# Optimization experiments

Hardware: AMD Instinct MI355X
Metric: run time of the kernel (lower is better)

The kernel has to match this reference:

```python
import jax, jax.numpy as jnp
import numpy as np
from jax import lax

NX, NY = 512, 512          # grid
NCHAN, NOPEN = 4, 16        # channels / MLP hidden
NT = 8                      # timesteps
CG_ITERS = 10               # fixed CG iterations (CG.pcg source unavailable)
H = 1.0 / 16.0
DT = 1.0 / 64.0
N = NX * NY


def apply_lap(u):
    """Weighted 5-point Laplacian (Sigma=1, Neumann BC) / h^2. u: (ny, nx)."""
    dx = u[:, 1:] - u[:, :-1]            # (ny, nx-1)
    dy = u[1:, :] - u[:-1, :]            # (ny-1, nx)
    out = jnp.zeros_like(u)
    out = out.at[:, :-1].add(-dx).at[:, 1:].add(dx)
    out = out.at[:-1, :].add(-dy).at[1:, :].add(dy)
    return out * (1.0 / (H * H))


def cg_solve(b, gamma):
    """Solve (L + gamma*I) x = b with x0=0, fixed CG iterations. b: (ny, nx)."""
    A = lambda v: apply_lap(v) + gamma * v
    x = jnp.zeros_like(b)
    r = b
    p = r
    rs = jnp.sum(r * r)

    def body(carry, _):
        x, r, p, rs = carry
        Ap = A(p)
        alpha = rs / jnp.sum(p * Ap)
        x = x + alpha * p
        r = r - alpha * Ap
        rs_new = jnp.sum(r * r)
        p = r + (rs_new / rs) * p
        return (x, r, p, rs_new), None

    (x, _, _, _), _ = lax.scan(body, (x, r, p, rs), None, length=CG_ITERS)
    return x


def setup_inputs() -> dict:
    key = jax.random.key(0)
    k0, k1, k2, k3 = jax.random.split(key, 4)
    U0 = jax.random.normal(k0, (N, NCHAN), dtype=jnp.float32)
    # xavier_normal_ init for the three MLP weights
    def xavier(k, shape):
        std = float(np.sqrt(2.0 / (shape[0] + shape[1])))
        return jax.random.normal(k, shape, dtype=jnp.float32) * std
    K1 = xavier(k1, (NCHAN, NOPEN))
    K2 = xavier(k2, (NOPEN, NOPEN))
    K3 = xavier(k3, (NOPEN, NCHAN))
    scale = jnp.array([0.001, 0.01, 0.1, 1.0], dtype=jnp.float32)
    return {"U0": U0, "scale": scale, "K1": K1, "K2": K2, "K3": K3}


def reference(U0, scale, K1, K2, K3):
    gamma = 1.0 / (scale * DT)  # (NCHAN,)

    def step(U, _):
        # implicit diffusion per channel: solve (L + g I) u_new = g * u
        grids = U.T.reshape(NCHAN, NY, NX)                       # (C, ny, nx)
        sol = jax.vmap(lambda g, gm: cg_solve(gm * g, gm))(grids, gamma)
        U = sol.reshape(NCHAN, N).T                              # (N, C)
        # reaction: 3-layer tanh MLP
        U = U + DT * jnp.tanh(jnp.tanh(jnp.tanh(U @ K1) @ K2) @ K3)
        return U, None

    U, _ = lax.scan(step, U0, None, length=NT)
    return U
```

## Files before the change

### kernel.cpp

```cpp
#include <hip/hip_runtime.h>

#define NXg 512
#define NYg 512
#define NNg (NXg*NYg)
#define TPB 512
#define NBT 256
#define NSTEPS 8
#define CGIT 10
#define DTf (1.0f/64.0f)
#define H2I 256.0f

#define RELGEN 4096
#define SCAL   4098
#define CTRL_FLOATS 8192
#define W_OFF(par,c) (CTRL_FLOATS + ((par)*4+(c))*NNg)
#define B_OFF(c)     (CTRL_FLOATS + (8+(c))*NNg)

__device__ __forceinline__ int ld_flag(int* p){
  return __hip_atomic_load(p, __ATOMIC_RELAXED, __HIP_MEMORY_SCOPE_AGENT);
}
__device__ __forceinline__ void st_flag(int* p, int v){
  __hip_atomic_store(p, v, __ATOMIC_RELAXED, __HIP_MEMORY_SCOPE_AGENT);
}
union F2U { unsigned long long u; float2 f; };
__device__ __forceinline__ float2 ldg2(float* p){
  F2U t; t.u = __hip_atomic_load((unsigned long long*)p, __ATOMIC_RELAXED, __HIP_MEMORY_SCOPE_AGENT);
  return t.f;
}
__device__ __forceinline__ void stg2(float* p, float2 v){
  F2U t; t.f = v;
  __hip_atomic_store((unsigned long long*)p, t.u, __ATOMIC_RELAXED, __HIP_MEMORY_SCOPE_AGENT);
}

__device__ __forceinline__ void mlp_all(const float* sW, const float* vv, float* o){
  float h1[16];
  #pragma unroll
  for (int h=0;h<16;++h)
    h1[h] = tanhf(vv[0]*sW[h]+vv[1]*sW[16+h]+vv[2]*sW[32+h]+vv[3]*sW[48+h]);
  o[0]=o[1]=o[2]=o[3]=0.f;
  #pragma unroll
  for (int j=0;j<16;++j){
    float s=0.f;
    #pragma unroll
    for (int h=0;h<16;++h) s += h1[h]*sW[64+16*h+j];
    const float t = tanhf(s);
    o[0]+=t*sW[320+4*j+0]; o[1]+=t*sW[320+4*j+1];
    o[2]+=t*sW[320+4*j+2]; o[3]+=t*sW[320+4*j+3];
  }
}

__global__ void __launch_bounds__(TPB)
drk(const float* __restrict__ U0, const float* __restrict__ scale,
    const float* __restrict__ K1, const float* __restrict__ K2,
    const float* __restrict__ K3, float* __restrict__ out,
    float* __restrict__ ws)
{
  __shared__ float sW[384];
  __shared__ float sP[2][4][NXg];
  __shared__ float wRed[8][12];
  __shared__ float sAB[8];

  const int tid=threadIdx.x, bid=blockIdx.x;
  const int r    = tid>>8;
  const int lane = tid&63;
  const int wv   = tid>>6;
  const int c2   = (tid&255)*2;
  const int grow = bid*2 + r;
  const int cell0= grow*NXg + c2;
  const bool hUp = (r==0) && (grow>0);
  const bool hDn = (r==1) && (grow<NYg-1);
  const bool hasHalo = hUp || hDn;
  const int hrow = (r==0) ? (grow-1) : (grow+1);

  if (tid < 384){
    float w;
    if (tid < 64)       w = K1[tid];
    else if (tid < 320) w = K2[tid-64];
    else                w = K3[tid-320];
    sW[tid]=w;
  }
  __syncthreads();

  int* wsi = (int*)ws;
  float gam[4];
  #pragma unroll
  for (int c=0;c<4;++c) gam[c] = 1.0f/(scale[c]*DTf);

  float xnew[2][4];
  {
    const float4 u0 = ((const float4*)U0)[cell0];
    const float4 u1 = ((const float4*)U0)[cell0+1];
    xnew[0][0]=u0.x; xnew[0][1]=u0.y; xnew[0][2]=u0.z; xnew[0][3]=u0.w;
    xnew[1][0]=u1.x; xnew[1][1]=u1.y; xnew[1][2]=u1.z; xnew[1][3]=u1.w;
  }

  float rs_prev[4]={0,0,0,0}, pAp_prev[4]={0,0,0,0};

  for (int step=0; step<NSTEPS; ++step){
    float rr[2][4], xx[2][4], pp[2][4], Ap[2][4];
    float rh[2][4], Aph[2][4];
    #pragma unroll
    for (int c=0;c<4;++c)
    #pragma unroll
    for (int k=0;k<2;++k){
      rr[k][c] = gam[c]*xnew[k][c];
      xx[k][c]=0.f; pp[k][c]=0.f; Ap[k][c]=0.f; Aph[k][c]=0.f; rh[k][c]=0.f;
    }
    if (hasHalo){
      if (step==0){
        const float4 h0 = ((const float4*)U0)[hrow*NXg + c2];
        const float4 h1 = ((const float4*)U0)[hrow*NXg + c2+1];
        rh[0][0]=gam[0]*h0.x; rh[0][1]=gam[1]*h0.y; rh[0][2]=gam[2]*h0.z; rh[0][3]=gam[3]*h0.w;
        rh[1][0]=gam[0]*h1.x; rh[1][1]=gam[1]*h1.y; rh[1][2]=gam[2]*h1.z; rh[1][3]=gam[3]*h1.w;
      } else {
        #pragma unroll
        for (int c=0;c<4;++c){
          const float2 h = ldg2(ws + B_OFF(c) + hrow*NXg + c2);
          rh[0][c]=h.x; rh[1][c]=h.y;
        }
      }
    }

    for (int it=0; it<CGIT; ++it){
      const int tgt = step*11 + it + 1;
      const int par = it&1;

      #pragma unroll
      for (int k=0;k<2;++k)
      #pragma unroll
      for (int c=0;c<4;++c) sP[r][c][c2+k] = rr[k][c];
      __syncthreads();

      float w[2][4];
      #pragma unroll
      for (int c=0;c<4;++c)
      #pragma unroll
      for (int k=0;k<2;++k){
        const int col = c2+k;
        const float u = rr[k][c];
        float s = 0.f;
        if (r==1) s += u - sP[0][c][col]; else if (grow>0)     s += u - rh[k][c];
        if (r==0) s += u - sP[1][c][col]; else if (grow<NYg-1) s += u - rh[k][c];
        if (col > 0)     s += u - ((k==1) ? rr[0][c] : sP[r][c][col-1]);
        if (col < NXg-1) s += u - ((k==0) ? rr[1][c] : sP[r][c][col+1]);
        w[k][c] = s*H2I + gam[c]*u;
      }
      if (hasHalo && it < CGIT-1){
        #pragma unroll
        for (int c=0;c<4;++c)
          stg2(ws + W_OFF(par,c) + grow*NXg + c2, make_float2(w[0][c],w[1][c]));
      }

      float m12[12];
      #pragma unroll
      for (int c=0;c<4;++c){
        float rs_l=0.f, rw_l=0.f, rA_l=0.f;
        #pragma unroll
        for (int k=0;k<2;++k){
          rs_l += rr[k][c]*rr[k][c];
          rw_l += rr[k][c]*w[k][c];
          rA_l += rr[k][c]*Ap[k][c];
        }
        m12[c]=rs_l; m12[4+c]=rw_l; m12[8+c]=rA_l;
      }
      #pragma unroll
      for (int m=0;m<12;++m){
        float v=m12[m];
        #pragma unroll
        for (int off=32; off; off>>=1) v += __shfl_xor(v, off);
        m12[m]=v;
      }
      if (lane==0){
        #pragma unroll
        for (int m=0;m<12;++m) wRed[wv][m]=m12[m];
      }
      asm volatile("s_waitcnt vmcnt(0)" ::: "memory");
      __syncthreads();

      if (wv==0){
        float s=0.f;
        if (lane<12){
          #pragma unroll
          for (int q=0;q<8;++q) s += wRed[q][lane];
        }
        const float s0 = __shfl(s, 2*lane);
        const float s1 = __shfl(s, 2*lane+1);
        if (lane<6) stg2(ws + bid*16 + 2*lane, make_float2(s0,s1));
        asm volatile("s_waitcnt vmcnt(0)" ::: "memory");
        if (lane==0) st_flag(&wsi[bid*16+12], tgt);
      }

      if (bid==0 && tid<64){
        const int b0 = tid*4;
        int ok=0;
        while(!ok){
          int m=1;
          #pragma unroll
          for (int j=0;j<4;++j) m &= (ld_flag(&wsi[(b0+j)*16+12]) >= tgt);
          ok=__all(m);
          if(!ok) __builtin_amdgcn_s_sleep(1);
        }
        float mm[12];
        #pragma unroll
        for (int m=0;m<12;++m) mm[m]=0.f;
        #pragma unroll
        for (int j=0;j<4;++j)
          #pragma unroll
          for (int t=0;t<6;++t){
            const float2 v = ldg2(ws + (b0+j)*16 + 2*t);
            mm[2*t] += v.x; mm[2*t+1] += v.y;
          }
        #pragma unroll
        for (int m=0;m<12;++m){
          float v=mm[m];
          #pragma unroll
          for (int off=32; off; off>>=1) v += __shfl_xor(v, off);
          mm[m]=v;
        }
        float aR[4], bR[4];
        #pragma unroll
        for (int c=0;c<4;++c){
          const float rsv=mm[c], rwv=mm[4+c], rAv=mm[8+c];
          const float bet = (it==0) ? 0.f
                          : ((rs_prev[c] > 0.f) ? rsv/rs_prev[c] : 0.f);
          const float pap = rwv + 2.f*bet*rAv + bet*bet*pAp_prev[c];
          const float alp = (rsv > 0.f && pap > 0.f) ? rsv/pap : 0.f;
          rs_prev[c]=rsv; pAp_prev[c]=pap;
          aR[c]=alp; bR[c]=bet;
        }
        if (tid==0){
          stg2(ws+SCAL+0, make_float2(aR[0],aR[1]));
          stg2(ws+SCAL+2, make_float2(aR[2],aR[3]));
          stg2(ws+SCAL+4, make_float2(bR[0],bR[1]));
          stg2(ws+SCAL+6, make_float2(bR[2],bR[3]));
          asm volatile("s_waitcnt vmcnt(0)" ::: "memory");
          st_flag(&wsi[RELGEN], tgt);
          #pragma unroll
          for (int c=0;c<4;++c){ sAB[c]=aR[c]; sAB[4+c]=bR[c]; }
        }
      } else if (bid!=0 && tid==0){
        while(ld_flag(&wsi[RELGEN]) < tgt) __builtin_amdgcn_s_sleep(1);
        const float2 a01=ldg2(ws+SCAL+0), a23=ldg2(ws+SCAL+2);
        const float2 b01=ldg2(ws+SCAL+4), b23=ldg2(ws+SCAL+6);
        sAB[0]=a01.x; sAB[1]=a01.y; sAB[2]=a23.x; sAB[3]=a23.y;
        sAB[4]=b01.x; sAB[5]=b01.y; sAB[6]=b23.x; sAB[7]=b23.y;
      }
      __syncthreads();
      float alpha[4], beta[4];
      #pragma unroll
      for (int c=0;c<4;++c){ alpha[c]=sAB[c]; beta[c]=sAB[4+c]; }

      #pragma unroll
      for (int k=0;k<2;++k)
      #pragma unroll
      for (int c=0;c<4;++c){
        pp[k][c] = rr[k][c] + beta[c]*pp[k][c];
        Ap[k][c] = w[k][c]  + beta[c]*Ap[k][c];
        xx[k][c] += alpha[c]*pp[k][c];
      }
      if (it < CGIT-1){
        #pragma unroll
        for (int k=0;k<2;++k)
        #pragma unroll
        for (int c=0;c<4;++c) rr[k][c] -= alpha[c]*Ap[k][c];
        if (hasHalo){
          #pragma unroll
          for (int c=0;c<4;++c){
            const float2 hw = ldg2(ws + W_OFF(par,c) + hrow*NXg + c2);
            Aph[0][c] = hw.x + beta[c]*Aph[0][c];
            Aph[1][c] = hw.y + beta[c]*Aph[1][c];
            rh[0][c] -= alpha[c]*Aph[0][c];
            rh[1][c] -= alpha[c]*Aph[1][c];
          }
        }
      }
      __syncthreads();
    }

    #pragma unroll
    for (int k=0;k<2;++k){
      float vv[4] = {xx[k][0], xx[k][1], xx[k][2], xx[k][3]};
      float o[4];
      mlp_all(sW, vv, o);
      #pragma unroll
      for (int c=0;c<4;++c) xnew[k][c] = xx[k][c] + DTf*tanhf(o[c]);
    }

    if (step < NSTEPS-1){
      const int tgt = step*11 + 11;
      if (hasHalo){
        #pragma unroll
        for (int c=0;c<4;++c)
          stg2(ws + B_OFF(c) + grow*NXg + c2,
               make_float2(gam[c]*xnew[0][c], gam[c]*xnew[1][c]));
      }
      asm volatile("s_waitcnt vmcnt(0)" ::: "memory");
      __syncthreads();
      if (tid==0) st_flag(&wsi[bid*16+12], tgt);
      if (bid==0 && tid<64){
        const int b0 = tid*4;
        int ok=0;
        while(!ok){
          int m=1;
          #pragma unroll
          for (int j=0;j<4;++j) m &= (ld_flag(&wsi[(b0+j)*16+12]) >= tgt);
          ok=__all(m);
          if(!ok) __builtin_amdgcn_s_sleep(1);
        }
        if (tid==0) st_flag(&wsi[RELGEN], tgt);
      } else if (bid!=0 && tid==0){
        while(ld_flag(&wsi[RELGEN]) < tgt) __builtin_amdgcn_s_sleep(1);
      }
      __syncthreads();
    } else {
      ((float4*)out)[cell0]   = make_float4(xnew[0][0],xnew[0][1],xnew[0][2],xnew[0][3]);
      ((float4*)out)[cell0+1] = make_float4(xnew[1][0],xnew[1][1],xnew[1][2],xnew[1][3]);
    }
  }
}

__global__ void diag_ws(float* out){ out[0] = 54321.0f; }

extern "C" void kernel_launch(void* const* d_in, const int* in_sizes, int n_in,
                              void* d_out, int out_size, void* d_ws, size_t ws_size,
                              hipStream_t stream) {
  const float* U0    = (const float*)d_in[0];
  const float* scale = (const float*)d_in[1];
  const float* K1    = (const float*)d_in[2];
  const float* K2    = (const float*)d_in[3];
  const float* K3    = (const float*)d_in[4];
  float* out = (float*)d_out;
  float* ws  = (float*)d_ws;

  const size_t need = (size_t)(CTRL_FLOATS + 12*NNg) * sizeof(float);
  if (ws_size < need) {
    hipLaunchKernelGGL(diag_ws, dim3(1), dim3(1), 0, stream, out);
    return;
  }
  hipMemsetAsync(ws, 0, CTRL_FLOATS*sizeof(float), stream);
  hipLaunchKernelGGL(drk, dim3(NBT), dim3(TPB), 0, stream,
                     U0, scale, K1, K2, K3, out, ws);
}
```

Before: 1.430 ms.

## Move grid-wide CG scalar reduction to a dedicated coordinator block with per-lane broadcast slots

```diff
diff --git a/kernel.cpp b/kernel.cpp
--- a/kernel.cpp
+++ b/kernel.cpp
@@ -4,14 +4,15 @@
 #define NYg 512
 #define NNg (NXg*NYg)
 #define TPB 512
-#define NBT 256
+#define NBC 256
+#define NBT 257
 #define NSTEPS 8
 #define CGIT 10
 #define DTf (1.0f/64.0f)
 #define H2I 256.0f
-
-#define RELGEN 4096
-#define SCAL   4098
+#define SPIN_LIM (1<<22)
+
+#define BC_OFF 4096
 #define CTRL_FLOATS 8192
 #define W_OFF(par,c) (CTRL_FLOATS + ((par)*4+(c))*NNg)
 #define B_OFF(c)     (CTRL_FLOATS + (8+(c))*NNg)
@@ -49,18 +50,88 @@
   }
 }
 
-__global__ void __launch_bounds__(TPB)
+__global__ void __launch_bounds__(TPB, 4)
 drk(const float* __restrict__ U0, const float* __restrict__ scale,
     const float* __restrict__ K1, const float* __restrict__ K2,
     const float* __restrict__ K3, float* __restrict__ out,
     float* __restrict__ ws)
 {
+  int* wsi = (int*)ws;
+  const int tid=threadIdx.x, bid=blockIdx.x;
+
+  if (bid == NBC){
+    if (tid >= 64) return;
+    const int lane = tid;
+    const int b0 = lane*4;
+    float* bc = ws + BC_OFF + lane*16;
+    float rs_prev[4]={0,0,0,0}, pAp_prev[4]={0,0,0,0};
+    for (int step=0; step<NSTEPS; ++step){
+      for (int it=0; it<CGIT; ++it){
+        const int tgt = step*11 + it + 1;
+        int ok=0, guard=0;
+        while(!ok && guard<SPIN_LIM){
+          int m=1;
+          #pragma unroll
+          for (int j=0;j<4;++j) m &= (ld_flag(&wsi[(b0+j)*16+12]) >= tgt);
+          ok=__all(m);
+          if(!ok){ __builtin_amdgcn_s_sleep(1); ++guard; }
+        }
+        float mm[12];
+        #pragma unroll
+        for (int m=0;m<12;++m) mm[m]=0.f;
+        #pragma unroll
+        for (int j=0;j<4;++j)
+          #pragma unroll
+          for (int t=0;t<6;++t){
+            const float2 v = ldg2(ws + (b0+j)*16 + 2*t);
+            mm[2*t] += v.x; mm[2*t+1] += v.y;
+          }
+        #pragma unroll
+        for (int m=0;m<12;++m){
+          float v=mm[m];
+          #pragma unroll
+          for (int off=32; off; off>>=1) v += __shfl_xor(v, off);
+          mm[m]=v;
+        }
+        float aR[4], bR[4];
+        #pragma unroll
+        for (int c=0;c<4;++c){
+          const float rsv=mm[c], rwv=mm[4+c], rAv=mm[8+c];
+          const float bet = (it==0) ? 0.f
+                          : ((rs_prev[c] > 0.f) ? rsv/rs_prev[c] : 0.f);
+          const float pap = rwv + 2.f*bet*rAv + bet*bet*pAp_prev[c];
+          const float alp = (rsv > 0.f && pap > 0.f) ? rsv/pap : 0.f;
+          rs_prev[c]=rsv; pAp_prev[c]=pap;
+          aR[c]=alp; bR[c]=bet;
+        }
+        stg2(bc+0, make_float2(aR[0],aR[1]));
+        stg2(bc+2, make_float2(aR[2],aR[3]));
+        stg2(bc+4, make_float2(bR[0],bR[1]));
+        stg2(bc+6, make_float2(bR[2],bR[3]));
+        asm volatile("s_waitcnt vmcnt(0)" ::: "memory");
+        st_flag(&wsi[BC_OFF + lane*16 + 8], tgt);
+      }
+      if (step < NSTEPS-1){
+        const int tgt = step*11 + 11;
+        int ok=0, guard=0;
+        while(!ok && guard<SPIN_LIM){
+          int m=1;
+          #pragma unroll
+          for (int j=0;j<4;++j) m &= (ld_flag(&wsi[(b0+j)*16+12]) >= tgt);
+          ok=__all(m);
+          if(!ok){ __builtin_amdgcn_s_sleep(1); ++guard; }
+        }
+        st_flag(&wsi[BC_OFF + lane*16 + 8], tgt);
+      }
+    }
+    return;
+  }
+
   __shared__ float sW[384];
   __shared__ float sP[2][4][NXg];
   __shared__ float wRed[8][12];
   __shared__ float sAB[8];
 
-  const int tid=threadIdx.x, bid=blockIdx.x;
   const int r    = tid>>8;
   const int lane = tid&63;
   const int wv   = tid>>6;
@@ -71,6 +142,8 @@
   const bool hDn = (r==1) && (grow<NYg-1);
   const bool hasHalo = hUp || hDn;
   const int hrow = (r==0) ? (grow-1) : (grow+1);
+  int* genL = &wsi[BC_OFF + (bid&63)*16 + 8];
+  float* bcL = ws + BC_OFF + (bid&63)*16;
 
   if (tid < 384){
     float w;
@@ -81,7 +154,6 @@
   }
   __syncthreads();
 
-  int* wsi = (int*)ws;
   float gam[4];
   #pragma unroll
   for (int c=0;c<4;++c) gam[c] = 1.0f/(scale[c]*DTf);
@@ -93,8 +165,6 @@
     xnew[0][0]=u0.x; xnew[0][1]=u0.y; xnew[0][2]=u0.z; xnew[0][3]=u0.w;
     xnew[1][0]=u1.x; xnew[1][1]=u1.y; xnew[1][2]=u1.z; xnew[1][3]=u1.w;
   }
-
-  float rs_prev[4]={0,0,0,0}, pAp_prev[4]={0,0,0,0};
 
   for (int step=0; step<NSTEPS; ++step){
     float rr[2][4], xx[2][4], pp[2][4], Ap[2][4];
@@ -190,58 +260,11 @@
         if (lane==0) st_flag(&wsi[bid*16+12], tgt);
       }
 
-      if (bid==0 && tid<64){
-        const int b0 = tid*4;
-        int ok=0;
-        while(!ok){
-          int m=1;
-          #pragma unroll
-          for (int j=0;j<4;++j) m &= (ld_flag(&wsi[(b0+j)*16+12]) >= tgt);
-          ok=__all(m);
-          if(!ok) __builtin_amdgcn_s_sleep(1);
-        }
-        float mm[12];
-        #pragma unroll
-        for (int m=0;m<12;++m) mm[m]=0.f;
-        #pragma unroll
-        for (int j=0;j<4;++j)
-          #pragma unroll
-          for (int t=0;t<6;++t){
-            const float2 v = ldg2(ws + (b0+j)*16 + 2*t);
-            mm[2*t] += v.x; mm[2*t+1] += v.y;
-          }
-        #pragma unroll
-        for (int m=0;m<12;++m){
-          float v=mm[m];
-          #pragma unroll
-          for (int off=32; off; off>>=1) v += __shfl_xor(v, off);
-          mm[m]=v;
-        }
-        float aR[4], bR[4];
-        #pragma unroll
-        for (int c=0;c<4;++c){
-          const float rsv=mm[c], rwv=mm[4+c], rAv=mm[8+c];
-          const float bet = (it==0) ? 0.f
-                          : ((rs_prev[c] > 0.f) ? rsv/rs_prev[c] : 0.f);
-          const float pap = rwv + 2.f*bet*rAv + bet*bet*pAp_prev[c];
-          const float alp = (rsv > 0.f && pap > 0.f) ? rsv/pap : 0.f;
-          rs_prev[c]=rsv; pAp_prev[c]=pap;
-          aR[c]=alp; bR[c]=bet;
-        }
-        if (tid==0){
-          stg2(ws+SCAL+0, make_float2(aR[0],aR[1]));
-          stg2(ws+SCAL+2, make_float2(aR[2],aR[3]));
-          stg2(ws+SCAL+4, make_float2(bR[0],bR[1]));
-          stg2(ws+SCAL+6, make_float2(bR[2],bR[3]));
-          asm volatile("s_waitcnt vmcnt(0)" ::: "memory");
-          st_flag(&wsi[RELGEN], tgt);
-          #pragma unroll
-          for (int c=0;c<4;++c){ sAB[c]=aR[c]; sAB[4+c]=bR[c]; }
-        }
-      } else if (bid!=0 && tid==0){
-        while(ld_flag(&wsi[RELGEN]) < tgt) __builtin_amdgcn_s_sleep(1);
-        const float2 a01=ldg2(ws+SCAL+0), a23=ldg2(ws+SCAL+2);
-        const float2 b01=ldg2(ws+SCAL+4), b23=ldg2(ws+SCAL+6);
+      if (tid==0){
+        int guard=0;
+        while(ld_flag(genL) < tgt && guard<SPIN_LIM){ __builtin_amdgcn_s_sleep(1); ++guard; }
+        const float2 a01=ldg2(bcL+0), a23=ldg2(bcL+2);
+        const float2 b01=ldg2(bcL+4), b23=ldg2(bcL+6);
         sAB[0]=a01.x; sAB[1]=a01.y; sAB[2]=a23.x; sAB[3]=a23.y;
         sAB[4]=b01.x; sAB[5]=b01.y; sAB[6]=b23.x; sAB[7]=b23.y;
       }
@@ -297,19 +320,9 @@
       asm volatile("s_waitcnt vmcnt(0)" ::: "memory");
       __syncthreads();
       if (tid==0) st_flag(&wsi[bid*16+12], tgt);
-      if (bid==0 && tid<64){
-        const int b0 = tid*4;
-        int ok=0;
-        while(!ok){
-          int m=1;
-          #pragma unroll
-          for (int j=0;j<4;++j) m &= (ld_flag(&wsi[(b0+j)*16+12]) >= tgt);
-          ok=__all(m);
-          if(!ok) __builtin_amdgcn_s_sleep(1);
-        }
-        if (tid==0) st_flag(&wsi[RELGEN], tgt);
-      } else if (bid!=0 && tid==0){
-        while(ld_flag(&wsi[RELGEN]) < tgt) __builtin_amdgcn_s_sleep(1);
+      if (tid==0){
+        int guard=0;
+        while(ld_flag(genL) < tgt && guard<SPIN_LIM){ __builtin_amdgcn_s_sleep(1); ++guard; }
       }
       __syncthreads();
     } else {
```

Measured after the change: 2.100 ms. 1.47x slower.
